# Kernel tuning notes

Measured on AMD Instinct MI355X. Metric: run time of the kernel, lower is better.

Reference implementation:

```python
import jax, jax.numpy as jnp
import numpy as np

B, S, D, H = 2, 2048, 2048, 16
HD = D // H


def setup_inputs() -> dict:
    key = jax.random.key(0)
    ks = jax.random.split(key, 11)
    scale = 1.0 / np.sqrt(D)
    return {
        "query": jax.random.normal(ks[0], (B, S, D), jnp.float32),
        "key_": jax.random.normal(ks[1], (B, S, D), jnp.float32),
        "value": jax.random.normal(ks[2], (B, S, D), jnp.float32),
        "Wq": jax.random.normal(ks[3], (D, D), jnp.float32) * scale,
        "bq": jnp.zeros((D,), jnp.float32),
        "Wk": jax.random.normal(ks[4], (D, D), jnp.float32) * scale,
        "bk": jnp.zeros((D,), jnp.float32),
        "Wv": jax.random.normal(ks[5], (D, D), jnp.float32) * scale,
        "bv": jnp.zeros((D,), jnp.float32),
        "Wo": jax.random.normal(ks[6], (D, D), jnp.float32) * scale,
        "bo": jnp.zeros((D,), jnp.float32),
    }


def reference(query, key_, value, Wq, bq, Wk, bk, Wv, bv, Wo, bo):
    # Linear projections (torch Linear: x @ W.T + b)
    q = query @ Wq.T + bq   # [B,S,D]
    k = key_ @ Wk.T + bk
    v = value @ Wv.T + bv
    # split heads -> [B,H,S,HD]
    def split(x):
        return x.reshape(B, S, H, HD).transpose(0, 2, 1, 3)
    q, k, v = split(q), split(k), split(v)
    # scaled dot-product attention, full NxN softmax
    scores = jnp.einsum('bhqd,bhkd->bhqk', q, k) / jnp.sqrt(jnp.float32(HD))
    attn = jax.nn.softmax(scores, axis=-1)
    out = jnp.einsum('bhqk,bhkd->bhqd', attn, v)
    out = out.transpose(0, 2, 1, 3).reshape(B, S, D)
    return out @ Wo.T + bo
```

## Files before the change

kernel.cpp:

```cpp
#include <hip/hip_runtime.h>
#include <stdint.h>

#define B_  2
#define S_  2048
#define D_  2048
#define H_  16
#define HD_ 128
#define M_  (B_ * S_)

typedef unsigned short u16;
typedef __attribute__((ext_vector_type(8))) short bf16x8;
typedef __attribute__((ext_vector_type(4))) float f32x4;

__device__ __forceinline__ u16 f2bf(float f) {
  union { float f; unsigned u; } x; x.f = f;
  unsigned r = x.u + 0x7fffu + ((x.u >> 16) & 1u);
  return (u16)(r >> 16);
}
__device__ __forceinline__ void gload16(const void* g, void* l) {
  __builtin_amdgcn_global_load_lds(
      (const __attribute__((address_space(1))) void*)g,
      (__attribute__((address_space(3))) void*)l, 16, 0, 0);
}
__device__ __forceinline__ void store_out(u16* p, float v)  { *p = f2bf(v); }
__device__ __forceinline__ void store_out(float* p, float v){ *p = v; }

struct CvtArgs {
  const float* src[7];
  u16* dst[7];
  int n8[7];
};
__global__ void __launch_bounds__(256)
cvt_all(CvtArgs a) {
  const int seg = blockIdx.y;
  const float* __restrict__ src = a.src[seg];
  u16* __restrict__ dst = a.dst[seg];
  const int n8 = a.n8[seg];
  int idx = blockIdx.x * 256 + threadIdx.x;
  const int stride = gridDim.x * 256;
  for (int i = idx; i < n8; i += stride) {
    f32x4 x = ((const f32x4*)src)[2 * i];
    f32x4 y = ((const f32x4*)src)[2 * i + 1];
    bf16x8 o;
    o[0] = (short)f2bf(x[0]); o[1] = (short)f2bf(x[1]);
    o[2] = (short)f2bf(x[2]); o[3] = (short)f2bf(x[3]);
    o[4] = (short)f2bf(y[0]); o[5] = (short)f2bf(y[1]);
    o[6] = (short)f2bf(y[2]); o[7] = (short)f2bf(y[3]);
    ((bf16x8*)dst)[i] = o;
  }
}

template <typename OT, bool BM>
__global__ void __launch_bounds__(512, 2)
gemm_nt_bias(const u16* __restrict__ A, const u16* __restrict__ W,
             const float* __restrict__ bias, OT* __restrict__ C,
             int M, int N, int K, float oscale, int lognbx) {
  __shared__ u16 lds[3 * 24576];

  const int tid  = threadIdx.x;
  const int lane = tid & 63;
  const int wave = tid >> 6;
  const int wm = wave >> 1;
  const int wn = wave & 1;
  const int lr = lane & 15;
  const int lg = lane >> 4;

  const int bid = blockIdx.x;
  const int cpx = gridDim.x >> 3;
  const int swz = (bid & 7) * cpx + (bid >> 3);
  const int m0 = (swz & ((1 << lognbx) - 1)) << 8;
  const int n0 = (swz >> lognbx) << 7;

  const f32x4 zero4 = {0.f, 0.f, 0.f, 0.f};
  f32x4 acc[4][4];
#pragma unroll
  for (int i = 0; i < 4; i++)
#pragma unroll
    for (int j = 0; j < 4; j++) acc[i][j] = zero4;

  size_t aoff[4];
#pragma unroll
  for (int i = 0; i < 4; i++) {
    const int c = i * 512 + tid;
    const int row = c >> 3;
    const int cc = (c & 7) ^ (row & 7);
    aoff[i] = (size_t)(m0 + row) * K + cc * 8;
  }
  size_t boff[2];
#pragma unroll
  for (int i = 0; i < 2; i++) {
    const int c = i * 512 + tid;
    const int row = c >> 3;
    const int cc = (c & 7) ^ (row & 7);
    boff[i] = (size_t)(n0 + row) * K + cc * 8;
  }

  u16* b0 = lds;
  u16* b1 = lds + 24576;
  u16* b2 = lds + 49152;

#define STAGE(buf, t)                                                     \
  do {                                                                    \
    const int k0s = (t) * 64;                                             \
    gload16(A + aoff[0] + k0s, (buf) + tid * 8);                          \
    gload16(A + aoff[1] + k0s, (buf) + 4096 + tid * 8);                   \
    gload16(A + aoff[2] + k0s, (buf) + 8192 + tid * 8);                   \
    gload16(A + aoff[3] + k0s, (buf) + 12288 + tid * 8);                  \
    gload16(W + boff[0] + k0s, (buf) + 16384 + tid * 8);                  \
    gload16(W + boff[1] + k0s, (buf) + 20480 + tid * 8);                  \
  } while (0)

  const int nt = K >> 6;
  STAGE(b0, 0);
  STAGE(b1, 1);

  for (int t = 0; t < nt; ++t) {
    if (t + 1 < nt) {
      asm volatile("s_waitcnt vmcnt(6)" ::: "memory");
    } else {
      asm volatile("s_waitcnt vmcnt(0)" ::: "memory");
    }
    __builtin_amdgcn_sched_barrier(0);
    __builtin_amdgcn_s_barrier();

    if (t + 2 < nt) STAGE(b2, t + 2);

#pragma unroll
    for (int ks = 0; ks < 2; ks++) {
      bf16x8 af[4], bfv[4];
#pragma unroll
      for (int mi = 0; mi < 4; mi++) {
        const int row = wm * 64 + mi * 16 + lr;
        const int pos = (ks * 4 + lg) ^ (row & 7);
        af[mi] = *(const bf16x8*)&b0[row * 64 + pos * 8];
      }
#pragma unroll
      for (int ni = 0; ni < 4; ni++) {
        const int row = wn * 64 + ni * 16 + lr;
        const int pos = (ks * 4 + lg) ^ (row & 7);
        bfv[ni] = *(const bf16x8*)&b0[16384 + row * 64 + pos * 8];
      }
      __builtin_amdgcn_s_setprio(1);
#pragma unroll
      for (int mi = 0; mi < 4; mi++)
#pragma unroll
        for (int ni = 0; ni < 4; ni++)
          acc[mi][ni] = __builtin_amdgcn_mfma_f32_16x16x32_bf16(
              af[mi], bfv[ni], acc[mi][ni], 0, 0, 0);
      __builtin_amdgcn_s_setprio(0);
    }

    u16* tmp = b0; b0 = b1; b1 = b2; b2 = tmp;
  }
#undef STAGE

  const int rbase = (lane >> 4) * 4;
#pragma unroll
  for (int ni = 0; ni < 4; ni++) {
    const int n = n0 + wn * 64 + ni * 16 + lr;
    float bv = 0.f;
    if (!BM) bv = bias[n];
#pragma unroll
    for (int mi = 0; mi < 4; mi++) {
#pragma unroll
      for (int j = 0; j < 4; j++) {
        const int m = m0 + wm * 64 + mi * 16 + rbase + j;
        const float bm = BM ? bias[m] : bv;
        store_out(&C[(size_t)m * N + n], (acc[mi][ni][j] + bm) * oscale);
      }
    }
  }
}

__global__ void __launch_bounds__(512)
flash_attn(const u16* __restrict__ Q, const u16* __restrict__ K,
           const u16* __restrict__ VT, u16* __restrict__ O) {
  __shared__ u16 Klds[64 * 128];
  __shared__ u16 VTlds[128 * 64];
  __shared__ u16 Plds[8][32 * 64];

  const int tid  = threadIdx.x;
  const int lane = tid & 63;
  const int wave = tid >> 6;
  const int lr = lane & 15;
  const int lk = (lane >> 4) * 8;
  const int rbase = (lane >> 4) * 4;

  const int bid = blockIdx.x;
  const int swz = (bid & 7) * 32 + (bid >> 3);
  const int qblk = swz & 7;
  const int bh   = swz >> 3;
  const int b = bh >> 4, h = bh & 15;
  const size_t base   = (size_t)b * S_ * D_ + (size_t)h * HD_;
  const size_t vtbase = (size_t)h * HD_ * M_ + (size_t)b * S_;
  const int q0 = qblk * 256 + wave * 32;

  bf16x8 qf[2][4];
#pragma unroll
  for (int qb = 0; qb < 2; qb++)
#pragma unroll
    for (int c = 0; c < 4; c++)
      qf[qb][c] = *(const bf16x8*)
          &Q[base + (size_t)(q0 + qb * 16 + lr) * D_ + c * 32 + lk];

  const f32x4 zero4 = {0.f, 0.f, 0.f, 0.f};
  f32x4 of[2][8];
#pragma unroll
  for (int qb = 0; qb < 2; qb++)
#pragma unroll
    for (int c = 0; c < 8; c++) of[qb][c] = zero4;
  float lrow[2][4] = {{0.f,0.f,0.f,0.f},{0.f,0.f,0.f,0.f}};

  const int kr0 = tid >> 4, kdc = (tid & 15) * 8;
  const int vr0 = tid >> 3, vsc = (tid & 7) * 8;

  bf16x8 kreg[2], vreg[2];
#pragma unroll
  for (int t = 0; t < 2; t++) {
    kreg[t] = *(const bf16x8*)&K[base + (size_t)(kr0 + 32 * t) * D_ + kdc];
    vreg[t] = *(const bf16x8*)&VT[vtbase + (size_t)(vr0 + 64 * t) * M_ + vsc];
  }

  for (int kb0 = 0; kb0 < S_; kb0 += 64) {
    __syncthreads();
#pragma unroll
    for (int t = 0; t < 2; t++) {
      const int krow = kr0 + 32 * t;
      *(bf16x8*)&Klds[krow * 128 + (kdc ^ ((krow & 7) << 3))] = kreg[t];
      const int vrow = vr0 + 64 * t;
      *(bf16x8*)&VTlds[vrow * 64 + (vsc ^ ((vrow & 7) << 3))] = vreg[t];
    }
    __syncthreads();

    if (kb0 + 64 < S_) {
      const int kn = kb0 + 64;
#pragma unroll
      for (int t = 0; t < 2; t++) {
        kreg[t] = *(const bf16x8*)&K[base + (size_t)(kn + kr0 + 32 * t) * D_ + kdc];
        vreg[t] = *(const bf16x8*)&VT[vtbase + (size_t)(vr0 + 64 * t) * M_ + kn + vsc];
      }
    }

    f32x4 s[2][4];
#pragma unroll
    for (int qb = 0; qb < 2; qb++)
#pragma unroll
      for (int kc = 0; kc < 4; kc++) s[qb][kc] = zero4;
    __builtin_amdgcn_s_setprio(1);
#pragma unroll
    for (int c = 0; c < 4; c++) {
#pragma unroll
      for (int kc = 0; kc < 4; kc++) {
        const int krow = kc * 16 + lr;
        bf16x8 kf = *(const bf16x8*)
            &Klds[krow * 128 + ((c * 32 + lk) ^ ((krow & 7) << 3))];
        s[0][kc] = __builtin_amdgcn_mfma_f32_16x16x32_bf16(qf[0][c], kf, s[0][kc], 0, 0, 0);
        s[1][kc] = __builtin_amdgcn_mfma_f32_16x16x32_bf16(qf[1][c], kf, s[1][kc], 0, 0, 0);
      }
    }
    __builtin_amdgcn_s_setprio(0);

#pragma unroll
    for (int qb = 0; qb < 2; qb++) {
#pragma unroll
      for (int j = 0; j < 4; j++) {
        float p0 = __builtin_amdgcn_exp2f(s[qb][0][j]);
        float p1 = __builtin_amdgcn_exp2f(s[qb][1][j]);
        float p2 = __builtin_amdgcn_exp2f(s[qb][2][j]);
        float p3 = __builtin_amdgcn_exp2f(s[qb][3][j]);
        lrow[qb][j] += (p0 + p1) + (p2 + p3);
        const int prow = qb * 16 + rbase + j;
        const int pb = prow * 64;
        const int sw = (prow & 7) << 3;
        Plds[wave][pb + ((     lr) ^ sw)] = f2bf(p0);
        Plds[wave][pb + ((16 + lr) ^ sw)] = f2bf(p1);
        Plds[wave][pb + ((32 + lr) ^ sw)] = f2bf(p2);
        Plds[wave][pb + ((48 + lr) ^ sw)] = f2bf(p3);
      }
    }

    __builtin_amdgcn_s_setprio(1);
#pragma unroll
    for (int h2 = 0; h2 < 2; h2++) {
      bf16x8 pa[2];
#pragma unroll
      for (int qb = 0; qb < 2; qb++) {
        const int prow = qb * 16 + lr;
        pa[qb] = *(const bf16x8*)
            &Plds[wave][prow * 64 + ((h2 * 32 + lk) ^ ((prow & 7) << 3))];
      }
#pragma unroll
      for (int c = 0; c < 8; c++) {
        const int vrow = c * 16 + lr;
        bf16x8 vf = *(const bf16x8*)
            &VTlds[vrow * 64 + ((h2 * 32 + lk) ^ ((vrow & 7) << 3))];
        of[0][c] = __builtin_amdgcn_mfma_f32_16x16x32_bf16(pa[0], vf, of[0][c], 0, 0, 0);
        of[1][c] = __builtin_amdgcn_mfma_f32_16x16x32_bf16(pa[1], vf, of[1][c], 0, 0, 0);
      }
    }
    __builtin_amdgcn_s_setprio(0);
  }

#pragma unroll
  for (int qb = 0; qb < 2; qb++) {
    float rinv[4];
#pragma unroll
    for (int j = 0; j < 4; j++) {
      float rs = lrow[qb][j];
      rs += __shfl_xor(rs, 1);
      rs += __shfl_xor(rs, 2);
      rs += __shfl_xor(rs, 4);
      rs += __shfl_xor(rs, 8);
      rinv[j] = 1.0f / rs;
    }
#pragma unroll
    for (int c = 0; c < 8; c++)
#pragma unroll
      for (int j = 0; j < 4; j++)
        O[base + (size_t)(q0 + qb * 16 + rbase + j) * D_ + c * 16 + lr] =
            f2bf(of[qb][c][j] * rinv[j]);
  }
}

extern "C" void kernel_launch(void* const* d_in, const int* in_sizes, int n_in,
                              void* d_out, int out_size, void* d_ws, size_t ws_size,
                              hipStream_t stream) {
  const float* query = (const float*)d_in[0];
  const float* key_  = (const float*)d_in[1];
  const float* value = (const float*)d_in[2];
  const float* Wq = (const float*)d_in[3];
  const float* bq = (const float*)d_in[4];
  const float* Wk = (const float*)d_in[5];
  const float* bk = (const float*)d_in[6];
  const float* Wv = (const float*)d_in[7];
  const float* bv = (const float*)d_in[8];
  const float* Wo = (const float*)d_in[9];
  const float* bo = (const float*)d_in[10];
  float* out = (float*)d_out;

  const size_t act = (size_t)M_ * D_;
  const size_t wsz = (size_t)D_ * D_;

  u16* p = (u16*)d_ws;
  u16* qb = p;  p += act;
  u16* kb = p;  p += act;
  u16* vb = p;  p += act;
  u16* wqb = p; p += wsz;
  u16* wkb = p; p += wsz;
  u16* wvb = p; p += wsz;
  u16* wob = p; p += wsz;
  u16* Qp  = p; p += act;
  u16* Kp  = p; p += act;
  u16* VpT = p; p += act;
  u16* AO  = p; p += act;

  dim3 blk(256);
  {
    CvtArgs a;
    a.src[0] = query; a.dst[0] = qb;  a.n8[0] = (int)(act / 8);
    a.src[1] = key_;  a.dst[1] = kb;  a.n8[1] = (int)(act / 8);
    a.src[2] = value; a.dst[2] = vb;  a.n8[2] = (int)(act / 8);
    a.src[3] = Wq;    a.dst[3] = wqb; a.n8[3] = (int)(wsz / 8);
    a.src[4] = Wk;    a.dst[4] = wkb; a.n8[4] = (int)(wsz / 8);
    a.src[5] = Wv;    a.dst[5] = wvb; a.n8[5] = (int)(wsz / 8);
    a.src[6] = Wo;    a.dst[6] = wob; a.n8[6] = (int)(wsz / 8);
    hipLaunchKernelGGL(cvt_all, dim3(512, 7), blk, 0, stream, a);
  }

  const float qscale = 1.4426950408889634f / 11.313708498984761f;

  dim3 g1(256);
  dim3 blk512(512);
  hipLaunchKernelGGL((gemm_nt_bias<u16, false>), g1, blk512, 0, stream,
                     qb, wqb, bq, Qp, M_, D_, D_, qscale, 4);
  hipLaunchKernelGGL((gemm_nt_bias<u16, false>), g1, blk512, 0, stream,
                     kb, wkb, bk, Kp, M_, D_, D_, 1.0f, 4);
  hipLaunchKernelGGL((gemm_nt_bias<u16, true>), g1, blk512, 0, stream,
                     wvb, vb, bv, VpT, D_, M_, D_, 1.0f, 3);

  hipLaunchKernelGGL(flash_attn, dim3(256), blk512, 0, stream, Qp, Kp, VpT, AO);

  hipLaunchKernelGGL((gemm_nt_bias<float, false>), g1, blk512, 0, stream,
                     AO, wob, bo, out, M_, D_, D_, 1.0f, 4);
}
```

Baseline: 263.6 us.

## Load GEMM A-fragments directly to registers, stage only W tile in LDS

The GEMM now reads each wave's A operand fragments straight from global memory into registers, with a one-tile register prefetch, and stages only the W tile through a single LDS buffer using plain register stores. This replaces the triple-buffered global_load_lds pipeline. The block-to-tile swizzle also changes so that consecutive blocks walk along N instead of M. The intent is to cut LDS traffic and footprint. The cost is that A rows are no longer shared between the two waves with the same wm, which doubles those global reads. There are also two __syncthreads per K step with less asynchronous overlap, and register pressure rises.

```diff
diff --git a/kernel.cpp b/kernel.cpp
--- a/kernel.cpp
+++ b/kernel.cpp
@@ -16,11 +16,6 @@
   union { float f; unsigned u; } x; x.f = f;
   unsigned r = x.u + 0x7fffu + ((x.u >> 16) & 1u);
   return (u16)(r >> 16);
-}
-__device__ __forceinline__ void gload16(const void* g, void* l) {
-  __builtin_amdgcn_global_load_lds(
-      (const __attribute__((address_space(1))) void*)g,
-      (__attribute__((address_space(3))) void*)l, 16, 0, 0);
 }
 __device__ __forceinline__ void store_out(u16* p, float v)  { *p = f2bf(v); }
 __device__ __forceinline__ void store_out(float* p, float v){ *p = v; }
@@ -54,8 +49,8 @@
 __global__ void __launch_bounds__(512, 2)
 gemm_nt_bias(const u16* __restrict__ A, const u16* __restrict__ W,
              const float* __restrict__ bias, OT* __restrict__ C,
-             int M, int N, int K, float oscale, int lognbx) {
-  __shared__ u16 lds[3 * 24576];
+             int M, int N, int K, float oscale, int lognbn) {
+  __shared__ u16 blds[128 * 64];
 
   const int tid  = threadIdx.x;
   const int lane = tid & 63;
@@ -68,8 +63,8 @@
   const int bid = blockIdx.x;
   const int cpx = gridDim.x >> 3;
   const int swz = (bid & 7) * cpx + (bid >> 3);
-  const int m0 = (swz & ((1 << lognbx) - 1)) << 8;
-  const int n0 = (swz >> lognbx) << 7;
+  const int m0 = (swz >> lognbn) << 8;
+  const int n0 = (swz & ((1 << lognbn) - 1)) << 7;
 
   const f32x4 zero4 = {0.f, 0.f, 0.f, 0.f};
   f32x4 acc[4][4];
@@ -78,67 +73,49 @@
 #pragma unroll
     for (int j = 0; j < 4; j++) acc[i][j] = zero4;
 
-  size_t aoff[4];
-#pragma unroll
-  for (int i = 0; i < 4; i++) {
-    const int c = i * 512 + tid;
-    const int row = c >> 3;
-    const int cc = (c & 7) ^ (row & 7);
-    aoff[i] = (size_t)(m0 + row) * K + cc * 8;
-  }
-  size_t boff[2];
-#pragma unroll
-  for (int i = 0; i < 2; i++) {
-    const int c = i * 512 + tid;
-    const int row = c >> 3;
-    const int cc = (c & 7) ^ (row & 7);
-    boff[i] = (size_t)(n0 + row) * K + cc * 8;
-  }
-
-  u16* b0 = lds;
-  u16* b1 = lds + 24576;
-  u16* b2 = lds + 49152;
-
-#define STAGE(buf, t)                                                     \
-  do {                                                                    \
-    const int k0s = (t) * 64;                                             \
-    gload16(A + aoff[0] + k0s, (buf) + tid * 8);                          \
-    gload16(A + aoff[1] + k0s, (buf) + 4096 + tid * 8);                   \
-    gload16(A + aoff[2] + k0s, (buf) + 8192 + tid * 8);                   \
-    gload16(A + aoff[3] + k0s, (buf) + 12288 + tid * 8);                  \
-    gload16(W + boff[0] + k0s, (buf) + 16384 + tid * 8);                  \
-    gload16(W + boff[1] + k0s, (buf) + 20480 + tid * 8);                  \
-  } while (0)
+  const u16* aptr[8];
+#pragma unroll
+  for (int i = 0; i < 8; i++) {
+    const int mi = i & 3, ks = i >> 2;
+    aptr[i] = A + (size_t)(m0 + wm * 64 + mi * 16 + lr) * K + ks * 32 + lg * 8;
+  }
+
+  const int brow0 = tid >> 3,          bgk = tid & 7;
+  const int brow1 = (tid + 512) >> 3;
+  const u16* bptr0 = W + (size_t)(n0 + brow0) * K + bgk * 8;
+  const u16* bptr1 = W + (size_t)(n0 + brow1) * K + bgk * 8;
+  const int bdst0 = brow0 * 64 + (bgk ^ (brow0 & 7)) * 8;
+  const int bdst1 = brow1 * 64 + (bgk ^ (brow1 & 7)) * 8;
+
+  bf16x8 bs0 = *(const bf16x8*)bptr0;
+  bf16x8 bs1 = *(const bf16x8*)bptr1;
+  bf16x8 afc[8], afn[8];
+#pragma unroll
+  for (int i = 0; i < 8; i++) afc[i] = *(const bf16x8*)aptr[i];
 
   const int nt = K >> 6;
-  STAGE(b0, 0);
-  STAGE(b1, 1);
-
   for (int t = 0; t < nt; ++t) {
+    __syncthreads();
+    *(bf16x8*)&blds[bdst0] = bs0;
+    *(bf16x8*)&blds[bdst1] = bs1;
+    __syncthreads();
+
     if (t + 1 < nt) {
-      asm volatile("s_waitcnt vmcnt(6)" ::: "memory");
-    } else {
-      asm volatile("s_waitcnt vmcnt(0)" ::: "memory");
-    }
-    __builtin_amdgcn_sched_barrier(0);
-    __builtin_amdgcn_s_barrier();
-
-    if (t + 2 < nt) STAGE(b2, t + 2);
+      const int adv = (t + 1) * 64;
+      bs0 = *(const bf16x8*)(bptr0 + adv);
+      bs1 = *(const bf16x8*)(bptr1 + adv);
+#pragma unroll
+      for (int i = 0; i < 8; i++) afn[i] = *(const bf16x8*)(aptr[i] + adv);
+    }
 
 #pragma unroll
     for (int ks = 0; ks < 2; ks++) {
-      bf16x8 af[4], bfv[4];
-#pragma unroll
-      for (int mi = 0; mi < 4; mi++) {
-        const int row = wm * 64 + mi * 16 + lr;
-        const int pos = (ks * 4 + lg) ^ (row & 7);
-        af[mi] = *(const bf16x8*)&b0[row * 64 + pos * 8];
-      }
+      bf16x8 bfv[4];
 #pragma unroll
       for (int ni = 0; ni < 4; ni++) {
         const int row = wn * 64 + ni * 16 + lr;
         const int pos = (ks * 4 + lg) ^ (row & 7);
-        bfv[ni] = *(const bf16x8*)&b0[16384 + row * 64 + pos * 8];
+        bfv[ni] = *(const bf16x8*)&blds[row * 64 + pos * 8];
       }
       __builtin_amdgcn_s_setprio(1);
 #pragma unroll
@@ -146,13 +123,15 @@
 #pragma unroll
         for (int ni = 0; ni < 4; ni++)
           acc[mi][ni] = __builtin_amdgcn_mfma_f32_16x16x32_bf16(
-              af[mi], bfv[ni], acc[mi][ni], 0, 0, 0);
+              afc[ks * 4 + mi], bfv[ni], acc[mi][ni], 0, 0, 0);
       __builtin_amdgcn_s_setprio(0);
     }
 
-    u16* tmp = b0; b0 = b1; b1 = b2; b2 = tmp;
-  }
-#undef STAGE
+    if (t + 1 < nt) {
+#pragma unroll
+      for (int i = 0; i < 8; i++) afc[i] = afn[i];
+    }
+  }
 
   const int rbase = (lane >> 4) * 4;
 #pragma unroll
@@ -376,7 +355,7 @@
   hipLaunchKernelGGL((gemm_nt_bias<u16, false>), g1, blk512, 0, stream,
                      kb, wkb, bk, Kp, M_, D_, D_, 1.0f, 4);
   hipLaunchKernelGGL((gemm_nt_bias<u16, true>), g1, blk512, 0, stream,
-                     wvb, vb, bv, VpT, D_, M_, D_, 1.0f, 3);
+                     wvb, vb, bv, VpT, D_, M_, D_, 1.0f, 5);
 
   hipLaunchKernelGGL(flash_attn, dim3(256), blk512, 0, stream, Qp, Kp, VpT, AO);
 
```

Result: slower. 441.5 us (+67.5%).

## Fuse Q and K projection GEMMs into one launch with 256x256 tiles

Applied to the files above, without the earlier changes.

Adds a new GEMM kernel that computes both the Q and K projections in a single launch, with each half of the grid handling one projection. Each block computes a 256x256 output tile with a 64-wide K step, double buffered in 128KB of LDS, instead of the smaller tiles of the generic kernel. The intent is to raise arithmetic intensity per LDS/global load and to fill the GPU with 256 blocks in one launch rather than two launches of 256 smaller tiles. The cost is much higher register use (32 accumulators per wave) and large LDS per block, which limits occupancy; the kernel waits on vmcnt(0) every iteration, which may expose load latency.

```diff
diff --git a/kernel.cpp b/kernel.cpp
--- a/kernel.cpp
+++ b/kernel.cpp
@@ -172,6 +172,122 @@
   }
 }
 
+__global__ void __launch_bounds__(512, 2)
+gemm2_256(const u16* __restrict__ Aq, const u16* __restrict__ Wqw,
+          const float* __restrict__ bqv, u16* __restrict__ Cq, float osq,
+          const u16* __restrict__ Ak, const u16* __restrict__ Wkw,
+          const float* __restrict__ bkv, u16* __restrict__ Ck) {
+  __shared__ u16 lds[2 * 32768];
+
+  const int job = blockIdx.x >> 7;
+  const u16* __restrict__ A = job ? Ak : Aq;
+  const u16* __restrict__ W = job ? Wkw : Wqw;
+  const float* __restrict__ bias = job ? bkv : bqv;
+  u16* __restrict__ C = job ? Ck : Cq;
+  const float oscale = job ? 1.0f : osq;
+  const int K = D_, N = D_;
+
+  const int tid  = threadIdx.x;
+  const int lane = tid & 63;
+  const int wave = tid >> 6;
+  const int wm = wave >> 2;
+  const int wn = wave & 3;
+  const int lr = lane & 15;
+  const int lg = lane >> 4;
+
+  const int lbid = blockIdx.x & 127;
+  const int swz = (lbid & 7) * 16 + (lbid >> 3);
+  const int m0 = (swz & 15) << 8;
+  const int n0 = (swz >> 4) << 8;
+
+  const f32x4 zero4 = {0.f, 0.f, 0.f, 0.f};
+  f32x4 acc[8][4];
+#pragma unroll
+  for (int i = 0; i < 8; i++)
+#pragma unroll
+    for (int j = 0; j < 4; j++) acc[i][j] = zero4;
+
+  size_t aoff[4], boff[4];
+#pragma unroll
+  for (int i = 0; i < 4; i++) {
+    const int c = i * 512 + tid;
+    const int row = c >> 3;
+    const int cc = (c & 7) ^ (row & 7);
+    aoff[i] = (size_t)(m0 + row) * K + cc * 8;
+    boff[i] = (size_t)(n0 + row) * K + cc * 8;
+  }
+
+  u16* cur = lds;
+  u16* nxt = lds + 32768;
+
+#define STAGE2(buf, t)                                                    \
+  do {                                                                    \
+    const int k0s = (t) * 64;                                             \
+    gload16(A + aoff[0] + k0s, (buf) + tid * 8);                          \
+    gload16(A + aoff[1] + k0s, (buf) + 4096 + tid * 8);                   \
+    gload16(A + aoff[2] + k0s, (buf) + 8192 + tid * 8);                   \
+    gload16(A + aoff[3] + k0s, (buf) + 12288 + tid * 8);                  \
+    gload16(W + boff[0] + k0s, (buf) + 16384 + tid * 8);                  \
+    gload16(W + boff[1] + k0s, (buf) + 20480 + tid * 8);                  \
+    gload16(W + boff[2] + k0s, (buf) + 24576 + tid * 8);                  \
+    gload16(W + boff[3] + k0s, (buf) + 28672 + tid * 8);                  \
+  } while (0)
+
+  const int nt = K >> 6;
+  STAGE2(cur, 0);
+
+  for (int t = 0; t < nt; ++t) {
+    asm volatile("s_waitcnt vmcnt(0)" ::: "memory");
+    __builtin_amdgcn_sched_barrier(0);
+    __builtin_amdgcn_s_barrier();
+
+    if (t + 1 < nt) STAGE2(nxt, t + 1);
+
+#pragma unroll
+    for (int ks = 0; ks < 2; ks++) {
+      bf16x8 af[8], bfv[4];
+#pragma unroll
+      for (int mi = 0; mi < 8; mi++) {
+        const int row = wm * 128 + mi * 16 + lr;
+        const int pos = (ks * 4 + lg) ^ (row & 7);
+        af[mi] = *(const bf16x8*)&cur[row * 64 + pos * 8];
+      }
+#pragma unroll
+      for (int ni = 0; ni < 4; ni++) {
+        const int row = wn * 64 + ni * 16 + lr;
+        const int pos = (ks * 4 + lg) ^ (row & 7);
+        bfv[ni] = *(const bf16x8*)&cur[16384 + row * 64 + pos * 8];
+      }
+      __builtin_amdgcn_s_setprio(1);
+#pragma unroll
+      for (int mi = 0; mi < 8; mi++)
+#pragma unroll
+        for (int ni = 0; ni < 4; ni++)
+          acc[mi][ni] = __builtin_amdgcn_mfma_f32_16x16x32_bf16(
+              af[mi], bfv[ni], acc[mi][ni], 0, 0, 0);
+      __builtin_amdgcn_s_setprio(0);
+    }
+
+    u16* tmp = cur; cur = nxt; nxt = tmp;
+  }
+#undef STAGE2
+
+  const int rbase = (lane >> 4) * 4;
+#pragma unroll
+  for (int ni = 0; ni < 4; ni++) {
+    const int n = n0 + wn * 64 + ni * 16 + lr;
+    const float bv = bias[n];
+#pragma unroll
+    for (int mi = 0; mi < 8; mi++) {
+#pragma unroll
+      for (int j = 0; j < 4; j++) {
+        const int m = m0 + wm * 128 + mi * 16 + rbase + j;
+        C[(size_t)m * N + n] = f2bf((acc[mi][ni][j] + bv) * oscale);
+      }
+    }
+  }
+}
+
 __global__ void __launch_bounds__(512)
 flash_attn(const u16* __restrict__ Q, const u16* __restrict__ K,
            const u16* __restrict__ VT, u16* __restrict__ O) {
@@ -371,10 +487,9 @@
 
   dim3 g1(256);
   dim3 blk512(512);
-  hipLaunchKernelGGL((gemm_nt_bias<u16, false>), g1, blk512, 0, stream,
-                     qb, wqb, bq, Qp, M_, D_, D_, qscale, 4);
-  hipLaunchKernelGGL((gemm_nt_bias<u16, false>), g1, blk512, 0, stream,
-                     kb, wkb, bk, Kp, M_, D_, D_, 1.0f, 4);
+  hipLaunchKernelGGL(gemm2_256, g1, blk512, 0, stream,
+                     qb, wqb, bq, Qp, qscale,
+                     kb, wkb, bk, Kp);
   hipLaunchKernelGGL((gemm_nt_bias<u16, true>), g1, blk512, 0, stream,
                      wvb, vb, bv, VpT, D_, M_, D_, 1.0f, 3);
 
```

After: 259.8 us. About the same (-1.4%).
